# Kernel optimization log

Measured on AMD Instinct MI355X. Metric: run time of the kernel, lower is better.

Reference implementation:

```python
import jax, jax.numpy as jnp
import numpy as np

N_NODES = 100000
IN_DIM = 512
HIDDEN = 64
NUM_CLASSES = 40
N_EDGES = 3200000


def setup_inputs() -> dict:
    key = jax.random.key(0)
    k1, k2, k3, k4, k5 = jax.random.split(key, 5)
    x = jax.random.normal(k1, (N_NODES, IN_DIM), dtype=jnp.float32)
    edge_index = jax.random.randint(k2, (2, N_EDGES), 0, N_NODES, dtype=jnp.int64)
    # Glorot init like PyG GCNConv, zero bias
    s1 = (6.0 / (IN_DIM + HIDDEN)) ** 0.5
    W1 = jax.random.uniform(k3, (IN_DIM, HIDDEN), jnp.float32, -s1, s1)
    b1 = jnp.zeros((HIDDEN,), jnp.float32)
    s2 = (6.0 / (HIDDEN + NUM_CLASSES)) ** 0.5
    W2 = jax.random.uniform(k4, (HIDDEN, NUM_CLASSES), jnp.float32, -s2, s2)
    b2 = jnp.zeros((NUM_CLASSES,), jnp.float32)
    return {"x": x, "edge_index": edge_index, "W1": W1, "b1": b1, "W2": W2, "b2": b2}


def _gcn_norm(edge_index, num_nodes):
    # Add self-loops, compute symmetric normalization D^-1/2 A D^-1/2 (PyG GCNConv default).
    loop = jnp.arange(num_nodes, dtype=edge_index.dtype)
    src = jnp.concatenate([edge_index[0], loop])
    dst = jnp.concatenate([edge_index[1], loop])
    deg = jax.ops.segment_sum(jnp.ones_like(src, dtype=jnp.float32), dst, num_segments=num_nodes)
    dinv = jnp.where(deg > 0, jax.lax.rsqrt(deg), 0.0)
    norm = dinv[src] * dinv[dst]  # [E+N]
    return src, dst, norm


def _gcn_conv(x, src, dst, norm, W, b, num_nodes):
    h = x @ W                                # [N, F_out]
    msg = h[src] * norm[:, None]             # gather + scale, [E+N, F_out]
    out = jax.ops.segment_sum(msg, dst, num_segments=num_nodes)  # scatter-add
    return out + b


def reference(x, edge_index, W1, b1, W2, b2):
    n = x.shape[0]
    src, dst, norm = _gcn_norm(edge_index, n)
    h = _gcn_conv(x, src, dst, norm, W1, b1, n)
    h = jax.nn.relu(h)
    # F.dropout(training=False) is identity in eval mode
    h = _gcn_conv(h, src, dst, norm, W2, b2, n)
    return jax.nn.log_softmax(h, axis=1)
```

## Files before the change

### kernel.cpp

```cpp
#include <hip/hip_runtime.h>
#include <hip/hip_bf16.h>
#include <cmath>

#define NN 100000
#define IND 512
#define HID 64
#define NC  40
#define BWN 256
#define NBKT ((NN + BWN - 1) / BWN)
#define CAP  12288
#define NBIN_BLOCKS 200

typedef unsigned int uint32;
typedef unsigned short ushort;
using short8 = __attribute__((ext_vector_type(8))) short;
using f32x4  = __attribute__((ext_vector_type(4))) float;

__device__ inline float bf_lo(uint32 u) { return __uint_as_float(u << 16); }
__device__ inline float bf_hi(uint32 u) { return __uint_as_float(u & 0xFFFF0000u); }
__device__ inline uint32 f2bf(float f) {
    uint32 u = __float_as_uint(f);
    return (u + 0x7FFFu + ((u >> 16) & 1u)) >> 16;
}
__device__ inline uint32 pack2bf(float a, float b) { return f2bf(a) | (f2bf(b) << 16); }


__global__ __launch_bounds__(256) void wt_init_kernel(const float* __restrict__ W1,
                                                      ushort* __restrict__ w1t,
                                                      int* __restrict__ gcursor) {
    int id = blockIdx.x * blockDim.x + threadIdx.x;
    if (id < IND * HID) {
        int n = id & 63, k = id >> 6;
        w1t[(size_t)n * IND + k] = (ushort)f2bf(W1[(size_t)k * HID + n]);
    }
    if (id < NBKT) gcursor[id] = id * CAP;
}


__global__ __launch_bounds__(512) void bin_kernel(const int* __restrict__ src,
                                                  const int* __restrict__ dst,
                                                  int* __restrict__ gcursor,
                                                  int* __restrict__ packed, int E) {
    __shared__ int hist[NBKT], base[NBKT], cur[NBKT];
    int b = blockIdx.x, t = threadIdx.x;
    int epb = (E + gridDim.x - 1) / gridDim.x;
    int lo = b * epb;
    int hi = lo + epb; if (hi > E) hi = E;
    for (int i = t; i < NBKT; i += 512) { hist[i] = 0; cur[i] = 0; }
    __syncthreads();
    for (int e = lo + t; e < hi; e += 512) atomicAdd(&hist[dst[e] >> 8], 1);
    __syncthreads();
    for (int i = t; i < NBKT; i += 512)
        if (hist[i]) base[i] = atomicAdd(&gcursor[i], hist[i]);
    __syncthreads();
    for (int e = lo + t; e < hi; e += 512) {
        int d = dst[e], s = src[e];
        int bk = d >> 8;
        int pos = base[bk] + atomicAdd(&cur[bk], 1);
        packed[pos] = ((d & 255) << 17) | s;
    }
}


__global__ __launch_bounds__(256) void csr_bucket_kernel(const int* __restrict__ packed,
                                                         const int* __restrict__ gcursor,
                                                         int* __restrict__ rowptr,
                                                         int* __restrict__ rowend,
                                                         int* __restrict__ colx,
                                                         float* __restrict__ dinv) {
    __shared__ int hist[BWN], pfx[BWN], cur[BWN];
    int b = blockIdx.x, t = threadIdx.x;
    int nlo = b * BWN;
    int ncnt = NN - nlo; if (ncnt > BWN) ncnt = BWN;
    int ebeg = b * CAP, eend = gcursor[b];
    hist[t] = 0;
    __syncthreads();
    for (int e = ebeg + t; e < eend; e += 256) atomicAdd(&hist[packed[e] >> 17], 1);
    __syncthreads();
    int h = hist[t];
    pfx[t] = h;
    __syncthreads();
    for (int off = 1; off < 256; off <<= 1) {
        int u = (t >= off) ? pfx[t - off] : 0;
        __syncthreads();
        pfx[t] += u;
        __syncthreads();
    }
    int excl = pfx[t] - h;
    cur[t] = excl;
    int g = nlo + t;
    if (t < ncnt) {
        rowptr[g] = ebeg + excl;
        rowend[g] = ebeg + excl + h;
        dinv[g] = rsqrtf((float)(h + 1));
    }
    __syncthreads();
    for (int e = ebeg + t; e < eend; e += 256) {
        int p = packed[e];
        int dl = p >> 17;
        int s = p & 0x1FFFF;
        int pos = ebeg + atomicAdd(&cur[dl], 1);
        colx[pos] = s;
    }
}


__global__ __launch_bounds__(256) void gemm1_mfma(const float* __restrict__ x,
                                                  const ushort* __restrict__ w1t,
                                                  const float* __restrict__ dinv,
                                                  ushort* __restrict__ hs, int M) {
    __shared__ ushort As[64 * 64];
    __shared__ ushort Bs[64 * 64];
    char* Ab = (char*)As;
    char* Bb = (char*)Bs;

    int t = threadIdx.x;
    int row0 = blockIdx.x * 64;

    int srow = t >> 2;
    int klane = t & 3;
    int grow = row0 + srow; if (grow > M - 1) grow = M - 1;
    const float* xrow = x + (size_t)grow * IND;
    const char* wrow = (const char*)(w1t + (size_t)srow * IND);
    int swrow = srow * 128;
    int swx = (srow & 7) << 4;

    int l = t & 63;
    int w = t >> 6;
    int lr = l & 15;
    int lk = (l >> 4) * 16;
    int arow_b = (w * 16 + lr) * 128;
    int aswz = ((w * 16 + lr) & 7) << 4;

    f32x4 acc[4] = {};

    float4 rx[4]; uint2 rw[4];
#pragma unroll
    for (int i = 0; i < 4; ++i) {
        rx[i] = *(const float4*)(xrow + i * 16 + klane * 4);
        rw[i] = *(const uint2*)(wrow + i * 32 + klane * 8);
    }

    for (int k0 = 0; k0 < IND; k0 += 64) {
#pragma unroll
        for (int i = 0; i < 4; ++i) {
            int kb = i * 32 + klane * 8;
            uint2 pkd;
            pkd.x = pack2bf(rx[i].x, rx[i].y);
            pkd.y = pack2bf(rx[i].z, rx[i].w);
            *(uint2*)(Ab + swrow + (kb ^ swx)) = pkd;
            *(uint2*)(Bb + swrow + (kb ^ swx)) = rw[i];
        }
        __syncthreads();

        if (k0 + 64 < IND) {
#pragma unroll
            for (int i = 0; i < 4; ++i) {
                rx[i] = *(const float4*)(xrow + k0 + 64 + i * 16 + klane * 4);
                rw[i] = *(const uint2*)(wrow + (k0 + 64) * 2 + i * 32 + klane * 8);
            }
        }

        short8 a0 = *(const short8*)(Ab + arow_b + ((0 + lk) ^ aswz));
        short8 a1 = *(const short8*)(Ab + arow_b + ((64 + lk) ^ aswz));
#pragma unroll
        for (int ns = 0; ns < 4; ++ns) {
            int brow = ns * 16 + lr;
            int bswz = (brow & 7) << 4;
            short8 b0 = *(const short8*)(Bb + brow * 128 + ((0 + lk) ^ bswz));
            short8 b1 = *(const short8*)(Bb + brow * 128 + ((64 + lk) ^ bswz));
            acc[ns] = __builtin_amdgcn_mfma_f32_16x16x32_bf16(a0, b0, acc[ns], 0, 0, 0);
            acc[ns] = __builtin_amdgcn_mfma_f32_16x16x32_bf16(a1, b1, acc[ns], 0, 0, 0);
        }
        __syncthreads();
    }

    int rbase = row0 + w * 16 + (l >> 4) * 4;
    float dv[4];
#pragma unroll
    for (int j = 0; j < 4; ++j) dv[j] = (rbase + j < M) ? dinv[rbase + j] : 0.f;
#pragma unroll
    for (int ns = 0; ns < 4; ++ns) {
        int col = ns * 16 + lr;
#pragma unroll
        for (int j = 0; j < 4; ++j) {
            int row = rbase + j;
            if (row < M) hs[(size_t)row * HID + col] = (ushort)f2bf(acc[ns][j] * dv[j]);
        }
    }
}


__global__ __launch_bounds__(256) void agg1_fused(const uint32* __restrict__ hs,
                                                  const int* __restrict__ rowptr,
                                                  const int* __restrict__ rowend,
                                                  const int* __restrict__ colx,
                                                  const float* __restrict__ dinv,
                                                  const float* __restrict__ b1,
                                                  const float* __restrict__ W2,
                                                  uint32* __restrict__ h2b) {
    __shared__ float w2s[64][42];
    int t = threadIdx.x;
    for (int i = t; i < HID * NC; i += 256) {
        int k = i / NC, c = i - k * NC;
        w2s[k][c] = W2[i];
    }
    __syncthreads();

    int node = (blockIdx.x * blockDim.x + t) >> 5;
    int l = t & 31;
    if (node >= NN) return;
    int beg = rowptr[node], end = rowend[node];
    uint32 u = hs[(size_t)node * 32 + l];
    float a0 = bf_lo(u), a1 = bf_hi(u);
    int e = beg;
    int n8 = beg + ((end - beg) & ~7);
    for (; e < n8; e += 8) {
        int c[8];
#pragma unroll
        for (int j = 0; j < 8; ++j) c[j] = __builtin_nontemporal_load(&colx[e + j]);
        uint32 uu[8];
#pragma unroll
        for (int j = 0; j < 8; ++j) uu[j] = hs[(size_t)c[j] * 32 + l];
#pragma unroll
        for (int j = 0; j < 8; ++j) { a0 += bf_lo(uu[j]); a1 += bf_hi(uu[j]); }
    }
    for (; e < end; ++e) {
        uint32 ue = hs[(size_t)__builtin_nontemporal_load(&colx[e]) * 32 + l];
        a0 += bf_lo(ue); a1 += bf_hi(ue);
    }
    float d = dinv[node];
    float2 bb = *(const float2*)(b1 + 2 * l);
    float v0 = a0 * d + bb.x;
    float v1 = a1 * d + bb.y;
    v0 = v0 > 0.f ? v0 : 0.f;
    v1 = v1 > 0.f ? v1 : 0.f;

    float s0 = 0.f, s1 = 0.f;
#pragma unroll
    for (int k = 0; k < 32; ++k) {
        float u0 = __shfl(v0, k, 32);
        float u1 = __shfl(v1, k, 32);
        if (l < 20) {
            float2 wa = *(const float2*)&w2s[2 * k][2 * l];
            float2 wb = *(const float2*)&w2s[2 * k + 1][2 * l];
            s0 += u0 * wa.x + u1 * wb.x;
            s1 += u0 * wa.y + u1 * wb.y;
        }
    }
    if (l < 20)
        __builtin_nontemporal_store(pack2bf(s0 * d, s1 * d), &h2b[(size_t)node * 20 + l]);
}


__global__ __launch_bounds__(256) void agg2_kernel(const uint32* __restrict__ h2b,
                                                   const int* __restrict__ rowptr,
                                                   const int* __restrict__ rowend,
                                                   const int* __restrict__ colx,
                                                   const float* __restrict__ dinv,
                                                   const float* __restrict__ b2,
                                                   float* __restrict__ out) {
    int node = (blockIdx.x * blockDim.x + threadIdx.x) >> 5;
    int l = threadIdx.x & 31;
    if (node >= NN) return;
    bool act = l < 20;
    int beg = rowptr[node], end = rowend[node];
    float a0 = 0.f, a1 = 0.f;
    if (act) {
        uint32 u = h2b[(size_t)node * 20 + l];
        a0 = bf_lo(u); a1 = bf_hi(u);
    }
    int e = beg;
    int n8 = beg + ((end - beg) & ~7);
    for (; e < n8; e += 8) {
        int c[8];
#pragma unroll
        for (int j = 0; j < 8; ++j) c[j] = __builtin_nontemporal_load(&colx[e + j]);
        if (act) {
            uint32 uu[8];
#pragma unroll
            for (int j = 0; j < 8; ++j) uu[j] = h2b[(size_t)c[j] * 20 + l];
#pragma unroll
            for (int j = 0; j < 8; ++j) { a0 += bf_lo(uu[j]); a1 += bf_hi(uu[j]); }
        }
    }
    for (; e < end; ++e) {
        int c = __builtin_nontemporal_load(&colx[e]);
        if (act) {
            uint32 ue = h2b[(size_t)c * 20 + l];
            a0 += bf_lo(ue); a1 += bf_hi(ue);
        }
    }

    float d = dinv[node];
    float v0 = -INFINITY, v1 = -INFINITY;
    if (act) {
        float2 bb = *(const float2*)(b2 + 2 * l);
        v0 = a0 * d + bb.x;
        v1 = a1 * d + bb.y;
    }
    float m = fmaxf(v0, v1);
#pragma unroll
    for (int off = 16; off; off >>= 1) m = fmaxf(m, __shfl_xor(m, off));
    float s = act ? (expf(v0 - m) + expf(v1 - m)) : 0.f;
#pragma unroll
    for (int off = 16; off; off >>= 1) s += __shfl_xor(s, off);
    if (act) {
        float ls = logf(s);
        __builtin_nontemporal_store(v0 - m - ls, &out[(size_t)node * NC + 2 * l]);
        __builtin_nontemporal_store(v1 - m - ls, &out[(size_t)node * NC + 2 * l + 1]);
    }
}


extern "C" void kernel_launch(void* const* d_in, const int* in_sizes, int n_in,
                              void* d_out, int out_size, void* d_ws, size_t ws_size,
                              hipStream_t stream) {
    const float* x  = (const float*)d_in[0];
    const int* ei   = (const int*)d_in[1];
    const float* W1 = (const float*)d_in[2];
    const float* b1 = (const float*)d_in[3];
    const float* W2 = (const float*)d_in[4];
    const float* b2 = (const float*)d_in[5];
    float* out = (float*)d_out;

    const int E = in_sizes[1] / 2;
    const int* src = ei;
    const int* dst = ei + E;

    char* p = (char*)d_ws;
    size_t off = 0;
    auto carve = [&](size_t bytes) {
        void* q = p + off;
        off = (off + bytes + 255) & ~(size_t)255;
        return q;
    };
    int* gcursor  = (int*)carve((size_t)NBKT * 4);
    int* rowptr   = (int*)carve((size_t)NN * 4);
    int* rowend   = (int*)carve((size_t)NN * 4);
    float* dinv   = (float*)carve((size_t)NN * 4);
    ushort* w1t   = (ushort*)carve((size_t)IND * HID * 2);
    ushort* hs    = (ushort*)carve((size_t)NN * HID * 2);
    uint32* h2b   = (uint32*)carve((size_t)NN * 20 * 4);
    int* colx     = (int*)carve((size_t)NBKT * CAP * 4);
    int* packed   = (int*)carve((size_t)NBKT * CAP * 4);

    wt_init_kernel<<<(IND * HID + 255) / 256, 256, 0, stream>>>(W1, w1t, gcursor);
    bin_kernel<<<NBIN_BLOCKS, 512, 0, stream>>>(src, dst, gcursor, packed, E);
    csr_bucket_kernel<<<NBKT, 256, 0, stream>>>(packed, gcursor, rowptr, rowend, colx, dinv);
    gemm1_mfma<<<(NN + 63) / 64, 256, 0, stream>>>(x, w1t, dinv, hs, NN);
    agg1_fused<<<(NN * 32 + 255) / 256, 256, 0, stream>>>((const uint32*)hs, rowptr, rowend, colx, dinv, b1, W2, h2b);
    agg2_kernel<<<(NN * 32 + 255) / 256, 256, 0, stream>>>(h2b, rowptr, rowend, colx, dinv, b2, out);
}
```

Baseline: 316.0 us.

## Split layer-2 projection out of aggregation into a separate MFMA GEMM kernel

The second-layer projection (h @ W2) is removed from the first aggregation kernel, where it ran as a shuffle-based scalar loop against W2 held in LDS. The aggregation kernel now writes the post-ReLU hidden activations as bf16 to a new buffer. A new gemm2_mfma kernel then applies bf16 MFMA against a transposed, zero-padded W2, which is prepared in the weight-init kernel. This removes per-node shuffle and FMA work and the per-block LDS staging of W2, at the cost of an extra kernel launch and an extra round trip of the hidden activations through global memory.

```diff
diff --git a/kernel.cpp b/kernel.cpp
--- a/kernel.cpp
+++ b/kernel.cpp
@@ -26,12 +26,18 @@
 
 
 __global__ __launch_bounds__(256) void wt_init_kernel(const float* __restrict__ W1,
+                                                      const float* __restrict__ W2,
                                                       ushort* __restrict__ w1t,
+                                                      ushort* __restrict__ w2t,
                                                       int* __restrict__ gcursor) {
     int id = blockIdx.x * blockDim.x + threadIdx.x;
     if (id < IND * HID) {
         int n = id & 63, k = id >> 6;
         w1t[(size_t)n * IND + k] = (ushort)f2bf(W1[(size_t)k * HID + n]);
+    } else if (id < IND * HID + 48 * HID) {
+        int id2 = id - IND * HID;
+        int n = id2 >> 6, k = id2 & 63;
+        w2t[id2] = (n < NC) ? (ushort)f2bf(W2[(size_t)k * NC + n]) : (ushort)0;
     }
     if (id < NBKT) gcursor[id] = id * CAP;
 }
@@ -191,24 +197,15 @@
 }
 
 
-__global__ __launch_bounds__(256) void agg1_fused(const uint32* __restrict__ hs,
-                                                  const int* __restrict__ rowptr,
-                                                  const int* __restrict__ rowend,
-                                                  const int* __restrict__ colx,
-                                                  const float* __restrict__ dinv,
-                                                  const float* __restrict__ b1,
-                                                  const float* __restrict__ W2,
-                                                  uint32* __restrict__ h2b) {
-    __shared__ float w2s[64][42];
-    int t = threadIdx.x;
-    for (int i = t; i < HID * NC; i += 256) {
-        int k = i / NC, c = i - k * NC;
-        w2s[k][c] = W2[i];
-    }
-    __syncthreads();
-
-    int node = (blockIdx.x * blockDim.x + t) >> 5;
-    int l = t & 31;
+__global__ __launch_bounds__(256) void agg1_kernel(const uint32* __restrict__ hs,
+                                                   const int* __restrict__ rowptr,
+                                                   const int* __restrict__ rowend,
+                                                   const int* __restrict__ colx,
+                                                   const float* __restrict__ dinv,
+                                                   const float* __restrict__ b1,
+                                                   uint32* __restrict__ h1) {
+    int node = (blockIdx.x * blockDim.x + threadIdx.x) >> 5;
+    int l = threadIdx.x & 31;
     if (node >= NN) return;
     int beg = rowptr[node], end = rowend[node];
     uint32 u = hs[(size_t)node * 32 + l];
@@ -235,21 +232,47 @@
     float v1 = a1 * d + bb.y;
     v0 = v0 > 0.f ? v0 : 0.f;
     v1 = v1 > 0.f ? v1 : 0.f;
-
-    float s0 = 0.f, s1 = 0.f;
-#pragma unroll
-    for (int k = 0; k < 32; ++k) {
-        float u0 = __shfl(v0, k, 32);
-        float u1 = __shfl(v1, k, 32);
-        if (l < 20) {
-            float2 wa = *(const float2*)&w2s[2 * k][2 * l];
-            float2 wb = *(const float2*)&w2s[2 * k + 1][2 * l];
-            s0 += u0 * wa.x + u1 * wb.x;
-            s1 += u0 * wa.y + u1 * wb.y;
-        }
-    }
-    if (l < 20)
-        __builtin_nontemporal_store(pack2bf(s0 * d, s1 * d), &h2b[(size_t)node * 20 + l]);
+    __builtin_nontemporal_store(pack2bf(v0, v1), &h1[(size_t)node * 32 + l]);
+}
+
+
+__global__ __launch_bounds__(256) void gemm2_mfma(const ushort* __restrict__ h1,
+                                                  const ushort* __restrict__ w2t,
+                                                  const float* __restrict__ dinv,
+                                                  ushort* __restrict__ h2b, int M) {
+    int t = threadIdx.x;
+    int w = t >> 6, l = t & 63;
+    int lr = l & 15, lh = l >> 4;
+    int row0 = blockIdx.x * 64 + w * 16;
+    int arow = row0 + lr; if (arow > M - 1) arow = M - 1;
+    const ushort* hrow = h1 + (size_t)arow * HID;
+
+    f32x4 acc[3] = {};
+#pragma unroll
+    for (int ks = 0; ks < 2; ++ks) {
+        short8 a = *(const short8*)(hrow + ks * 32 + lh * 8);
+#pragma unroll
+        for (int ns = 0; ns < 3; ++ns) {
+            short8 b = *(const short8*)(w2t + (size_t)(ns * 16 + lr) * HID + ks * 32 + lh * 8);
+            acc[ns] = __builtin_amdgcn_mfma_f32_16x16x32_bf16(a, b, acc[ns], 0, 0, 0);
+        }
+    }
+
+    int rbase = row0 + lh * 4;
+    float dv[4];
+#pragma unroll
+    for (int j = 0; j < 4; ++j) dv[j] = (rbase + j < M) ? dinv[rbase + j] : 0.f;
+#pragma unroll
+    for (int ns = 0; ns < 3; ++ns) {
+        int col = ns * 16 + lr;
+        if (col < NC) {
+#pragma unroll
+            for (int j = 0; j < 4; ++j) {
+                int row = rbase + j;
+                if (row < M) h2b[(size_t)row * NC + col] = (ushort)f2bf(acc[ns][j] * dv[j]);
+            }
+        }
+    }
 }
 
 
@@ -340,15 +363,18 @@
     int* rowend   = (int*)carve((size_t)NN * 4);
     float* dinv   = (float*)carve((size_t)NN * 4);
     ushort* w1t   = (ushort*)carve((size_t)IND * HID * 2);
+    ushort* w2t   = (ushort*)carve((size_t)48 * HID * 2);
     ushort* hs    = (ushort*)carve((size_t)NN * HID * 2);
-    uint32* h2b   = (uint32*)carve((size_t)NN * 20 * 4);
+    uint32* h1    = (uint32*)carve((size_t)NN * 32 * 4);
+    ushort* h2b   = (ushort*)carve((size_t)NN * NC * 2);
     int* colx     = (int*)carve((size_t)NBKT * CAP * 4);
     int* packed   = (int*)carve((size_t)NBKT * CAP * 4);
 
-    wt_init_kernel<<<(IND * HID + 255) / 256, 256, 0, stream>>>(W1, w1t, gcursor);
+    wt_init_kernel<<<(IND * HID + 48 * HID + 255) / 256, 256, 0, stream>>>(W1, W2, w1t, w2t, gcursor);
     bin_kernel<<<NBIN_BLOCKS, 512, 0, stream>>>(src, dst, gcursor, packed, E);
     csr_bucket_kernel<<<NBKT, 256, 0, stream>>>(packed, gcursor, rowptr, rowend, colx, dinv);
     gemm1_mfma<<<(NN + 63) / 64, 256, 0, stream>>>(x, w1t, dinv, hs, NN);
-    agg1_fused<<<(NN * 32 + 255) / 256, 256, 0, stream>>>((const uint32*)hs, rowptr, rowend, colx, dinv, b1, W2, h2b);
-    agg2_kernel<<<(NN * 32 + 255) / 256, 256, 0, stream>>>(h2b, rowptr, rowend, colx, dinv, b2, out);
-}
+    agg1_kernel<<<(NN * 32 + 255) / 256, 256, 0, stream>>>((const uint32*)hs, rowptr, rowend, colx, dinv, b1, h1);
+    gemm2_mfma<<<(NN + 63) / 64, 256, 0, stream>>>((const ushort*)h1, w2t, dinv, h2b, NN);
+    agg2_kernel<<<(NN * 32 + 255) / 256, 256, 0, stream>>>((const uint32*)h2b, rowptr, rowend, colx, dinv, b2, out);
+}
```

Measured after the change: 290.1 us (median of 2 runs). 8.2% less time.
